# Kernel optimization log

Measured on AMD Instinct MI355X. Metric: run time of the kernel, lower is better.

The kernel has to match this reference:

```python
import jax, jax.numpy as jnp
import numpy as np

B, E, T = 8192, 512, 32


def setup_inputs() -> dict:
    key = jax.random.key(0)
    k1, k2, k3, k4, k5, k6 = jax.random.split(key, 6)
    s1 = 1.0 / np.sqrt(E)  # torch nn.Linear default init scale (uniform bound)
    return {
        "g_exp": jax.random.normal(k1, (B, E), dtype=jnp.float32),
        "tissue_vector": jax.random.randint(k2, (B, 1), 0, T, dtype=jnp.int64),
        # per-tissue head params: Linear(E,E) then Linear(E,1)
        "W1": jax.random.uniform(k3, (T, E, E), jnp.float32, -s1, s1),
        "b1": jax.random.uniform(k4, (T, E), jnp.float32, -s1, s1),
        "W2": jax.random.uniform(k5, (T, E), jnp.float32, -s1, s1),
        "b2": jax.random.uniform(k6, (T,), jnp.float32, -s1, s1),
    }


def reference(g_exp, tissue_vector, W1, b1, W2, b2):
    # Each sample b is routed through the MLP head of its tissue id.
    # Vectorized: run every sample through every tissue head, then select.
    # h[b,t,:] = GELU(g_exp[b] @ W1[t] + b1[t])
    h = jax.nn.gelu(jnp.einsum("be,teh->bth", g_exp, W1) + b1[None, :, :],
                    approximate=False)  # exact erf GELU, matches torch nn.GELU
    # y[b,t] = softplus(h[b,t] @ W2[t] + b2[t])   (Softplus since loss_fn='poisson')
    y = jax.nn.softplus(jnp.einsum("bth,th->bt", h, W2) + b2[None, :])
    tid = tissue_vector[:, 0]  # [B], tissue id per sample
    return jnp.take_along_axis(y, tid[:, None], axis=1)  # [B, 1]
```

## Files before the change

kernel.cpp:

```cpp
#include <hip/hip_runtime.h>
#include <math.h>

#define B_N 8192
#define E_N 512
#define T_N 32
#define DEPTH 5

typedef short bf16x8 __attribute__((ext_vector_type(8)));
typedef float f32x4 __attribute__((ext_vector_type(4)));

#define WS_OFFS   256
#define WS_RANK   512
#define WS_ORDER  33280
#define WS_YACC   66048
#define WS_ABF    98816
#define WS_W1T    (WS_ABF + 8388608)
#define WS_REQ    (WS_W1T + 33554432/2)

typedef __attribute__((address_space(1))) const unsigned int gas_u32;
typedef __attribute__((address_space(3))) unsigned int las_u32;

static __device__ __forceinline__ unsigned short f2bf(float f) {
    unsigned int u = __float_as_uint(f);
    unsigned int r = u + 0x7fffu + ((u >> 16) & 1u);
    return (unsigned short)(r >> 16);
}

__global__ __launch_bounds__(256) void k_pre(
    const float* __restrict__ W1, unsigned short* __restrict__ W1T,
    const float* __restrict__ g_exp, unsigned short* __restrict__ Abf,
    const int* __restrict__ tv, int* __restrict__ offs_g,
    int* __restrict__ rank, int* __restrict__ order, float* __restrict__ yacc) {
    int cid = blockIdx.x, tid = threadIdx.x;
    if (cid < 2048) {
        __shared__ float T[64][65];
        int t = cid >> 6, r = cid & 63;
        int k0 = (r >> 3) * 64, n0 = (r & 7) * 64;
        int g = tid >> 4, c = tid & 15;
#pragma unroll
        for (int p = 0; p < 4; ++p) {
            int row = p * 16 + g;
            float4 v = *(const float4*)(W1 + ((size_t)t * E_N + k0 + row) * E_N + n0 + c * 4);
            T[c * 4 + 0][row] = v.x;
            T[c * 4 + 1][row] = v.y;
            T[c * 4 + 2][row] = v.z;
            T[c * 4 + 3][row] = v.w;
        }
        __syncthreads();
#pragma unroll
        for (int p = 0; p < 4; ++p) {
            int n = p * 16 + g;
            ushort4 o;
            o.x = f2bf(T[n][c * 4 + 0]);
            o.y = f2bf(T[n][c * 4 + 1]);
            o.z = f2bf(T[n][c * 4 + 2]);
            o.w = f2bf(T[n][c * 4 + 3]);
            *(ushort4*)(W1T + ((size_t)t * E_N + n0 + n) * E_N + k0 + c * 4) = o;
        }
    } else if (cid < 2304) {
        int b0 = (cid - 2048) * 32;
#pragma unroll 4
        for (int pp = 0; pp < 16; ++pp) {
            int idx = pp * 256 + tid;
            int row = idx >> 7, c = idx & 127;
            float4 v = *(const float4*)(g_exp + ((size_t)(b0 + row)) * E_N + c * 4);
            ushort4 o;
            o.x = f2bf(v.x); o.y = f2bf(v.y); o.z = f2bf(v.z); o.w = f2bf(v.w);
            *(ushort4*)(Abf + ((size_t)(b0 + row)) * E_N + c * 4) = o;
        }
    } else {
        __shared__ int lh[4][32], wcur[4][32], offs_s[33];
        int w = tid >> 6;
        if (tid < 128) lh[tid >> 5][tid & 31] = 0;
        __syncthreads();
        int tval[32];
#pragma unroll
        for (int c = 0; c < 32; ++c) tval[c] = tv[c * 256 + tid];
#pragma unroll
        for (int c = 0; c < 32; ++c) atomicAdd(&lh[w][tval[c]], 1);
        __syncthreads();
        if (tid < 32) {
            int s = lh[0][tid] + lh[1][tid] + lh[2][tid] + lh[3][tid];
            int excl = 0;
#pragma unroll
            for (int i = 0; i < 32; ++i) {
                int v = __shfl(s, i, 64);
                if (i < tid) excl += v;
            }
            offs_s[tid] = excl;
            offs_g[tid] = excl;
            if (tid == 31) { offs_s[32] = excl + s; offs_g[32] = excl + s; }
        }
        __syncthreads();
        if (tid < 128) {
            int ww = tid >> 5, t = tid & 31;
            int s = offs_s[t];
            for (int w2 = 0; w2 < ww; ++w2) s += lh[w2][t];
            wcur[ww][t] = s;
        }
        __syncthreads();
#pragma unroll
        for (int c = 0; c < 32; ++c) {
            int b = c * 256 + tid;
            int pos = atomicAdd(&wcur[w][tval[c]], 1);
            rank[b] = pos;
            order[pos] = b;
        }
        float4 z = make_float4(0.f, 0.f, 0.f, 0.f);
#pragma unroll
        for (int c = 0; c < 8; ++c) *(float4*)(yacc + (c * 256 + tid) * 4) = z;
    }
}

__global__ __launch_bounds__(256) void k_gemm_mfma(
    const unsigned short* __restrict__ Abf, const unsigned short* __restrict__ W1T,
    const float* __restrict__ b1, const float* __restrict__ W2,
    const int* __restrict__ offs, const int* __restrict__ order,
    float* __restrict__ yacc) {
    int wi = blockIdx.x;
    int mt = wi >> 7;
    int rem = wi & 127;
    int t = rem >> 2, nt = rem & 3;
    int base = offs[t];
    int n_t = offs[t + 1] - base;
    int m0 = mt * 128;
    if (m0 >= n_t) return;
    int n0 = nt * 128;

    __shared__ __align__(16) unsigned short As[DEPTH][128 * 32];
    __shared__ __align__(16) unsigned short Bs[DEPTH][128 * 32];

    int tid = threadIdx.x;
    int wave = tid >> 6, lane = tid & 63;
    int quad = lane >> 4, l15 = lane & 15;
    int wm = (wave >> 1) * 64, wn = (wave & 1) * 64;

    int idx0 = tid, idx1 = tid + 256;
    int r0 = idx0 >> 2;
    int kc = (idx0 & 3) ^ (r0 & 3);
    int r1 = r0 + 64;
    int i0 = base + m0 + r0; if (i0 > B_N - 1) i0 = B_N - 1;
    int i1 = base + m0 + r1; if (i1 > B_N - 1) i1 = B_N - 1;
    int o0 = order[i0], o1 = order[i1];
    const unsigned short* pA0 = Abf + (size_t)o0 * E_N + kc * 8;
    const unsigned short* pA1 = Abf + (size_t)o1 * E_N + kc * 8;
    const unsigned short* pB0 = W1T + ((size_t)t * E_N + n0 + r0) * E_N + kc * 8;
    const unsigned short* pB1 = W1T + ((size_t)t * E_N + n0 + r1) * E_N + kc * 8;

    f32x4 acc[4][4];
#pragma unroll
    for (int mi = 0; mi < 4; ++mi)
#pragma unroll
        for (int ni = 0; ni < 4; ++ni) acc[mi][ni] = (f32x4){0.f, 0.f, 0.f, 0.f};

#define ISSUE(kk) do {                                                                              \
        __builtin_amdgcn_global_load_lds((gas_u32*)(pB0 + (kk) * 32),                               \
                                         (las_u32*)&Bs[(kk) % DEPTH][idx0 * 8], 16, 0, 0);          \
        __builtin_amdgcn_global_load_lds((gas_u32*)(pB1 + (kk) * 32),                               \
                                         (las_u32*)&Bs[(kk) % DEPTH][idx1 * 8], 16, 0, 0);          \
        __builtin_amdgcn_global_load_lds((gas_u32*)(pA0 + (kk) * 32),                               \
                                         (las_u32*)&As[(kk) % DEPTH][idx0 * 8], 16, 0, 0);          \
        __builtin_amdgcn_global_load_lds((gas_u32*)(pA1 + (kk) * 32),                               \
                                         (las_u32*)&As[(kk) % DEPTH][idx1 * 8], 16, 0, 0);          \
    } while (0)

    ISSUE(0); ISSUE(1); ISSUE(2); ISSUE(3);

    int aoff[4], boff[4];
#pragma unroll
    for (int i = 0; i < 4; ++i) {
        aoff[i] = ((wm + i * 16 + l15) * 4 + (quad ^ (l15 & 3))) * 8;
        boff[i] = ((wn + i * 16 + l15) * 4 + (quad ^ (l15 & 3))) * 8;
    }

#define STAGE(it, W) do {                                                                           \
        asm volatile("s_waitcnt vmcnt(%0)" :: "n"(W) : "memory");                                   \
        asm volatile("s_barrier" ::: "memory");                                                     \
        const unsigned short* Ab = &As[(it) % DEPTH][0];                                            \
        const unsigned short* Bb = &Bs[(it) % DEPTH][0];                                            \
        bf16x8 af[4], bfr[4];                                                                       \
        _Pragma("unroll") for (int i = 0; i < 4; ++i) {                                             \
            af[i]  = *(const bf16x8*)(Ab + aoff[i]);                                                \
            bfr[i] = *(const bf16x8*)(Bb + boff[i]);                                                \
        }                                                                                           \
        _Pragma("unroll") for (int mi = 0; mi < 4; ++mi)                                            \
            _Pragma("unroll") for (int ni = 0; ni < 4; ++ni)                                        \
                acc[mi][ni] = __builtin_amdgcn_mfma_f32_16x16x32_bf16(af[mi], bfr[ni],              \
                                                                      acc[mi][ni], 0, 0, 0);        \
        if ((it) + 4 < 16) ISSUE((it) + 4);                                                         \
    } while (0)

    STAGE(0, 12);  STAGE(1, 12);  STAGE(2, 12);  STAGE(3, 12);
    STAGE(4, 12);  STAGE(5, 12);  STAGE(6, 12);  STAGE(7, 12);
    STAGE(8, 12);  STAGE(9, 12);  STAGE(10, 12); STAGE(11, 12);
    STAGE(12, 12); STAGE(13, 8);  STAGE(14, 4);  STAGE(15, 0);
#undef STAGE
#undef ISSUE

    float pr[4][4];
#pragma unroll
    for (int mi = 0; mi < 4; ++mi)
#pragma unroll
        for (int r = 0; r < 4; ++r) pr[mi][r] = 0.f;
#pragma unroll
    for (int ni = 0; ni < 4; ++ni) {
        int n = n0 + wn + ni * 16 + l15;
        float bb = b1[t * E_N + n];
        float w2 = W2[t * E_N + n];
#pragma unroll
        for (int mi = 0; mi < 4; ++mi)
#pragma unroll
            for (int r = 0; r < 4; ++r) {
                float u = acc[mi][ni][r] + bb;
                float gg = 0.5f * u * (1.f + erff(u * 0.70710678118654752f));
                pr[mi][r] = fmaf(gg, w2, pr[mi][r]);
            }
    }
#pragma unroll
    for (int off = 1; off <= 8; off <<= 1)
#pragma unroll
        for (int mi = 0; mi < 4; ++mi)
#pragma unroll
            for (int r = 0; r < 4; ++r) pr[mi][r] += __shfl_xor(pr[mi][r], off, 64);

    if (l15 == 0) {
#pragma unroll
        for (int mi = 0; mi < 4; ++mi)
#pragma unroll
            for (int r = 0; r < 4; ++r) {
                int row = m0 + wm + mi * 16 + quad * 4 + r;
                if (row < n_t) atomicAdd(&yacc[base + row], pr[mi][r]);
            }
    }
}

__global__ void k_final(const float* __restrict__ yacc, const int* __restrict__ rank,
                        const int* __restrict__ tv, const float* __restrict__ b2,
                        float* __restrict__ out, int use_rank) {
    int b = blockIdx.x * blockDim.x + threadIdx.x;
    if (b < B_N) {
        int idx = use_rank ? rank[b] : b;
        float x = yacc[idx] + b2[tv[b]];
        out[b] = fmaxf(x, 0.f) + log1pf(expf(-fabsf(x)));
    }
}

__global__ __launch_bounds__(256) void k_prep_sb(
    const int* __restrict__ tv, int* __restrict__ offs_g,
    int* __restrict__ rank, int* __restrict__ order, float* __restrict__ yacc) {
    __shared__ int lh[4][32], wcur[4][32], offs_s[33];
    int tid = threadIdx.x, w = tid >> 6;
    if (tid < 128) lh[tid >> 5][tid & 31] = 0;
    __syncthreads();
    int tval[32];
#pragma unroll
    for (int c = 0; c < 32; ++c) tval[c] = tv[c * 256 + tid];
#pragma unroll
    for (int c = 0; c < 32; ++c) atomicAdd(&lh[w][tval[c]], 1);
    __syncthreads();
    if (tid < 32) {
        int s = lh[0][tid] + lh[1][tid] + lh[2][tid] + lh[3][tid];
        int excl = 0;
#pragma unroll
        for (int i = 0; i < 32; ++i) {
            int v = __shfl(s, i, 64);
            if (i < tid) excl += v;
        }
        offs_s[tid] = excl;
        offs_g[tid] = excl;
        if (tid == 31) { offs_s[32] = excl + s; offs_g[32] = excl + s; }
    }
    __syncthreads();
    if (tid < 128) {
        int ww = tid >> 5, t = tid & 31;
        int s = offs_s[t];
        for (int w2 = 0; w2 < ww; ++w2) s += lh[w2][t];
        wcur[ww][t] = s;
    }
    __syncthreads();
#pragma unroll
    for (int c = 0; c < 32; ++c) {
        int b = c * 256 + tid;
        int pos = atomicAdd(&wcur[w][tval[c]], 1);
        rank[b] = pos;
        order[pos] = b;
    }
    float4 z = make_float4(0.f, 0.f, 0.f, 0.f);
#pragma unroll
    for (int c = 0; c < 8; ++c) *(float4*)(yacc + (c * 256 + tid) * 4) = z;
}

__global__ __launch_bounds__(256) void fb_gemm(
    const float* __restrict__ g_exp, const float* __restrict__ W1,
    const float* __restrict__ b1, const float* __restrict__ W2,
    const int* __restrict__ offs, const int* __restrict__ order,
    float* __restrict__ yacc) {
    int t = blockIdx.z;
    int base = offs[t];
    int n_t = offs[t + 1] - base;
    int m0 = blockIdx.y * 64;
    if (m0 >= n_t) return;
    int n0 = blockIdx.x * 128;

    __shared__ float As[32][68];
    __shared__ float Bs[32][128];
    __shared__ int sidx[64];

    int tid = threadIdx.x;
    if (tid < 64) {
        int m = m0 + tid;
        sidx[tid] = (m < n_t) ? order[base + m] : -1;
    }
    __syncthreads();

    int ty = tid >> 4, tx = tid & 15;
    float acc[4][8];
#pragma unroll
    for (int r = 0; r < 4; ++r)
#pragma unroll
        for (int c = 0; c < 8; ++c) acc[r][c] = 0.f;

    for (int k0 = 0; k0 < E_N; k0 += 32) {
#pragma unroll
        for (int p = 0; p < 2; ++p) {
            int idx = tid + 256 * p;
            int row = idx >> 3, kcq = idx & 7;
            int s = sidx[row];
            float4 v = make_float4(0.f, 0.f, 0.f, 0.f);
            if (s >= 0) v = *(const float4*)(g_exp + (size_t)s * E_N + k0 + kcq * 4);
            As[kcq * 4 + 0][row] = v.x;
            As[kcq * 4 + 1][row] = v.y;
            As[kcq * 4 + 2][row] = v.z;
            As[kcq * 4 + 3][row] = v.w;
        }
#pragma unroll
        for (int p = 0; p < 4; ++p) {
            int idx = tid + 256 * p;
            int kr = idx >> 5, c4 = idx & 31;
            *(float4*)(&Bs[kr][c4 * 4]) =
                *(const float4*)(W1 + ((size_t)t * E_N + (k0 + kr)) * E_N + n0 + c4 * 4);
        }
        __syncthreads();
#pragma unroll
        for (int e = 0; e < 32; ++e) {
            float4 a = *(const float4*)(&As[e][ty * 4]);
            float4 bA = *(const float4*)(&Bs[e][tx * 4]);
            float4 bB = *(const float4*)(&Bs[e][tx * 4 + 64]);
            float av[4] = {a.x, a.y, a.z, a.w};
            float bv[8] = {bA.x, bA.y, bA.z, bA.w, bB.x, bB.y, bB.z, bB.w};
#pragma unroll
            for (int r = 0; r < 4; ++r)
#pragma unroll
                for (int c = 0; c < 8; ++c) acc[r][c] = fmaf(av[r], bv[c], acc[r][c]);
        }
        __syncthreads();
    }

    float pr[4] = {0.f, 0.f, 0.f, 0.f};
#pragma unroll
    for (int c = 0; c < 8; ++c) {
        int n = n0 + tx * 4 + ((c >= 4) ? 64 : 0) + (c & 3);
        float bb = b1[t * E_N + n];
        float w2 = W2[t * E_N + n];
#pragma unroll
        for (int r = 0; r < 4; ++r) {
            float u = acc[r][c] + bb;
            float g = 0.5f * u * (1.f + erff(u * 0.70710678118654752f));
            pr[r] = fmaf(g, w2, pr[r]);
        }
    }
#pragma unroll
    for (int off = 8; off >= 1; off >>= 1)
#pragma unroll
        for (int r = 0; r < 4; ++r) pr[r] += __shfl_xor(pr[r], off, 64);

    if (tx == 0) {
#pragma unroll
        for (int r = 0; r < 4; ++r) {
            int m = m0 + ty * 4 + r;
            if (m < n_t) atomicAdd(&yacc[sidx[ty * 4 + r]], pr[r]);
        }
    }
}

extern "C" void kernel_launch(void* const* d_in, const int* in_sizes, int n_in,
                              void* d_out, int out_size, void* d_ws, size_t ws_size,
                              hipStream_t stream) {
    const float* g_exp = (const float*)d_in[0];
    const int*   tv    = (const int*)d_in[1];
    const float* W1    = (const float*)d_in[2];
    const float* b1    = (const float*)d_in[3];
    const float* W2    = (const float*)d_in[4];
    const float* b2    = (const float*)d_in[5];
    float* out = (float*)d_out;

    char* ws = (char*)d_ws;
    int* offs   = (int*)(ws + WS_OFFS);
    int* rank   = (int*)(ws + WS_RANK);
    int* order  = (int*)(ws + WS_ORDER);
    float* yacc = (float*)(ws + WS_YACC);

    if (ws_size >= (size_t)WS_REQ) {
        unsigned short* Abf = (unsigned short*)(ws + WS_ABF);
        unsigned short* W1T = (unsigned short*)(ws + WS_W1T);
        k_pre<<<2305, 256, 0, stream>>>(W1, W1T, g_exp, Abf, tv, offs, rank, order, yacc);
        k_gemm_mfma<<<512, 256, 0, stream>>>(Abf, W1T, b1, W2, offs, order, yacc);
        k_final<<<32, 256, 0, stream>>>(yacc, rank, tv, b2, out, 1);
    } else {
        k_prep_sb<<<1, 256, 0, stream>>>(tv, offs, rank, order, yacc);
        fb_gemm<<<dim3(4, 8, 32), 256, 0, stream>>>(g_exp, W1, b1, W2, offs, order, yacc);
        k_final<<<32, 256, 0, stream>>>(yacc, rank, tv, b2, out, 0);
    }
}
```

Measured before the change: 133.3 us.

## Fuse activation bf16 conversion and tissue routing into the MFMA GEMM kernel

Removes the separate g_exp-to-bf16 conversion and the single-block histogram/sort stage from the preprocess kernel. Each GEMM block now counts its tissue's rows from tv itself, builds the row list in LDS, loads fp32 activations straight into LDS and converts them to bf16 when reading MFMA fragments. Per-column partial sums go to eight per-slab buffers with plain stores instead of atomics, and the final kernel reduces them, so the yacc zeroing is no longer needed. In exchange every block rescans all 8192 tissue ids, the A tile doubles in size (fp32), and pipeline depth drops from 5 to 3 buffers.

```diff
diff --git a/kernel.cpp b/kernel.cpp
--- a/kernel.cpp
+++ b/kernel.cpp
@@ -1,10 +1,10 @@
 #include <hip/hip_runtime.h>
+#include <hip/hip_bf16.h>
 #include <math.h>
 
 #define B_N 8192
 #define E_N 512
 #define T_N 32
-#define DEPTH 5
 
 typedef short bf16x8 __attribute__((ext_vector_type(8)));
 typedef float f32x4 __attribute__((ext_vector_type(4)));
@@ -13,9 +13,9 @@
 #define WS_RANK   512
 #define WS_ORDER  33280
 #define WS_YACC   66048
-#define WS_ABF    98816
-#define WS_W1T    (WS_ABF + 8388608)
-#define WS_REQ    (WS_W1T + 33554432/2)
+#define WS_YACC8  98816
+#define WS_W1T    360960
+#define WS_REQ    (WS_W1T + 16777216)
 
 typedef __attribute__((address_space(1))) const unsigned int gas_u32;
 typedef __attribute__((address_space(3))) unsigned int las_u32;
@@ -26,126 +26,103 @@
     return (unsigned short)(r >> 16);
 }
 
-__global__ __launch_bounds__(256) void k_pre(
-    const float* __restrict__ W1, unsigned short* __restrict__ W1T,
-    const float* __restrict__ g_exp, unsigned short* __restrict__ Abf,
-    const int* __restrict__ tv, int* __restrict__ offs_g,
-    int* __restrict__ rank, int* __restrict__ order, float* __restrict__ yacc) {
+static __device__ __forceinline__ unsigned int pk2(float a, float b) {
+    __hip_bfloat162 h = __float22bfloat162_rn(float2{a, b});
+    unsigned int u;
+    __builtin_memcpy(&u, &h, 4);
+    return u;
+}
+
+__global__ __launch_bounds__(256) void k_pre(const float* __restrict__ W1,
+                                             unsigned short* __restrict__ W1T) {
+    __shared__ float T[64][65];
     int cid = blockIdx.x, tid = threadIdx.x;
-    if (cid < 2048) {
-        __shared__ float T[64][65];
-        int t = cid >> 6, r = cid & 63;
-        int k0 = (r >> 3) * 64, n0 = (r & 7) * 64;
-        int g = tid >> 4, c = tid & 15;
-#pragma unroll
-        for (int p = 0; p < 4; ++p) {
-            int row = p * 16 + g;
-            float4 v = *(const float4*)(W1 + ((size_t)t * E_N + k0 + row) * E_N + n0 + c * 4);
-            T[c * 4 + 0][row] = v.x;
-            T[c * 4 + 1][row] = v.y;
-            T[c * 4 + 2][row] = v.z;
-            T[c * 4 + 3][row] = v.w;
-        }
-        __syncthreads();
-#pragma unroll
-        for (int p = 0; p < 4; ++p) {
-            int n = p * 16 + g;
-            ushort4 o;
-            o.x = f2bf(T[n][c * 4 + 0]);
-            o.y = f2bf(T[n][c * 4 + 1]);
-            o.z = f2bf(T[n][c * 4 + 2]);
-            o.w = f2bf(T[n][c * 4 + 3]);
-            *(ushort4*)(W1T + ((size_t)t * E_N + n0 + n) * E_N + k0 + c * 4) = o;
-        }
-    } else if (cid < 2304) {
-        int b0 = (cid - 2048) * 32;
-#pragma unroll 4
-        for (int pp = 0; pp < 16; ++pp) {
-            int idx = pp * 256 + tid;
-            int row = idx >> 7, c = idx & 127;
-            float4 v = *(const float4*)(g_exp + ((size_t)(b0 + row)) * E_N + c * 4);
-            ushort4 o;
-            o.x = f2bf(v.x); o.y = f2bf(v.y); o.z = f2bf(v.z); o.w = f2bf(v.w);
-            *(ushort4*)(Abf + ((size_t)(b0 + row)) * E_N + c * 4) = o;
-        }
-    } else {
-        __shared__ int lh[4][32], wcur[4][32], offs_s[33];
-        int w = tid >> 6;
-        if (tid < 128) lh[tid >> 5][tid & 31] = 0;
-        __syncthreads();
-        int tval[32];
-#pragma unroll
-        for (int c = 0; c < 32; ++c) tval[c] = tv[c * 256 + tid];
-#pragma unroll
-        for (int c = 0; c < 32; ++c) atomicAdd(&lh[w][tval[c]], 1);
-        __syncthreads();
-        if (tid < 32) {
-            int s = lh[0][tid] + lh[1][tid] + lh[2][tid] + lh[3][tid];
-            int excl = 0;
-#pragma unroll
-            for (int i = 0; i < 32; ++i) {
-                int v = __shfl(s, i, 64);
-                if (i < tid) excl += v;
-            }
-            offs_s[tid] = excl;
-            offs_g[tid] = excl;
-            if (tid == 31) { offs_s[32] = excl + s; offs_g[32] = excl + s; }
-        }
-        __syncthreads();
-        if (tid < 128) {
-            int ww = tid >> 5, t = tid & 31;
-            int s = offs_s[t];
-            for (int w2 = 0; w2 < ww; ++w2) s += lh[w2][t];
-            wcur[ww][t] = s;
-        }
-        __syncthreads();
-#pragma unroll
-        for (int c = 0; c < 32; ++c) {
-            int b = c * 256 + tid;
-            int pos = atomicAdd(&wcur[w][tval[c]], 1);
-            rank[b] = pos;
-            order[pos] = b;
-        }
-        float4 z = make_float4(0.f, 0.f, 0.f, 0.f);
-#pragma unroll
-        for (int c = 0; c < 8; ++c) *(float4*)(yacc + (c * 256 + tid) * 4) = z;
+    int t = cid >> 6, r = cid & 63;
+    int k0 = (r >> 3) * 64, n0 = (r & 7) * 64;
+    int g = tid >> 4, c = tid & 15;
+#pragma unroll
+    for (int p = 0; p < 4; ++p) {
+        int row = p * 16 + g;
+        float4 v = *(const float4*)(W1 + ((size_t)t * E_N + k0 + row) * E_N + n0 + c * 4);
+        T[c * 4 + 0][row] = v.x;
+        T[c * 4 + 1][row] = v.y;
+        T[c * 4 + 2][row] = v.z;
+        T[c * 4 + 3][row] = v.w;
+    }
+    __syncthreads();
+#pragma unroll
+    for (int p = 0; p < 4; ++p) {
+        int n = p * 16 + g;
+        ushort4 o;
+        o.x = f2bf(T[n][c * 4 + 0]);
+        o.y = f2bf(T[n][c * 4 + 1]);
+        o.z = f2bf(T[n][c * 4 + 2]);
+        o.w = f2bf(T[n][c * 4 + 3]);
+        *(ushort4*)(W1T + ((size_t)t * E_N + n0 + n) * E_N + k0 + c * 4) = o;
     }
 }
 
 __global__ __launch_bounds__(256) void k_gemm_mfma(
-    const unsigned short* __restrict__ Abf, const unsigned short* __restrict__ W1T,
-    const float* __restrict__ b1, const float* __restrict__ W2,
-    const int* __restrict__ offs, const int* __restrict__ order,
-    float* __restrict__ yacc) {
+    const float* __restrict__ g_exp, const unsigned short* __restrict__ W1T,
+    const int* __restrict__ tv, const float* __restrict__ b1,
+    const float* __restrict__ W2, float* __restrict__ yacc8) {
     int wi = blockIdx.x;
     int mt = wi >> 7;
     int rem = wi & 127;
     int t = rem >> 2, nt = rem & 3;
-    int base = offs[t];
-    int n_t = offs[t + 1] - base;
-    int m0 = mt * 128;
-    if (m0 >= n_t) return;
-    int n0 = nt * 128;
-
-    __shared__ __align__(16) unsigned short As[DEPTH][128 * 32];
-    __shared__ __align__(16) unsigned short Bs[DEPTH][128 * 32];
+    int m0 = mt * 128, n0 = nt * 128;
 
     int tid = threadIdx.x;
     int wave = tid >> 6, lane = tid & 63;
     int quad = lane >> 4, l15 = lane & 15;
     int wm = (wave >> 1) * 64, wn = (wave & 1) * 64;
 
-    int idx0 = tid, idx1 = tid + 256;
-    int r0 = idx0 >> 2;
-    int kc = (idx0 & 3) ^ (r0 & 3);
-    int r1 = r0 + 64;
-    int i0 = base + m0 + r0; if (i0 > B_N - 1) i0 = B_N - 1;
-    int i1 = base + m0 + r1; if (i1 > B_N - 1) i1 = B_N - 1;
-    int o0 = order[i0], o1 = order[i1];
-    const unsigned short* pA0 = Abf + (size_t)o0 * E_N + kc * 8;
-    const unsigned short* pA1 = Abf + (size_t)o1 * E_N + kc * 8;
-    const unsigned short* pB0 = W1T + ((size_t)t * E_N + n0 + r0) * E_N + kc * 8;
-    const unsigned short* pB1 = W1T + ((size_t)t * E_N + n0 + r1) * E_N + kc * 8;
+    __shared__ int wsum[4];
+    __shared__ int rows_s[128];
+
+    int tvals[32];
+    const int4* tvp = (const int4*)(tv + tid * 32);
+#pragma unroll
+    for (int j = 0; j < 8; ++j) ((int4*)tvals)[j] = tvp[j];
+    int myc = 0;
+#pragma unroll
+    for (int j = 0; j < 32; ++j) myc += (tvals[j] == t) ? 1 : 0;
+    int inc = myc;
+#pragma unroll
+    for (int o = 1; o < 64; o <<= 1) {
+        int u = __shfl_up(inc, o, 64);
+        if (lane >= o) inc += u;
+    }
+    if (lane == 63) wsum[wave] = inc;
+    if (tid < 128) rows_s[tid] = 0;
+    __syncthreads();
+    int n_t = wsum[0] + wsum[1] + wsum[2] + wsum[3];
+    if (m0 >= n_t) return;
+    int wbase = 0;
+    for (int i = 0; i < wave; ++i) wbase += wsum[i];
+    int rk = wbase + inc - myc;
+#pragma unroll
+    for (int j = 0; j < 32; ++j)
+        if (tvals[j] == t) {
+            int rr = rk++;
+            if (rr >= m0 && rr < m0 + 128) rows_s[rr - m0] = tid * 32 + j;
+        }
+    __syncthreads();
+
+    const unsigned short* Bsrc = W1T + ((size_t)t * E_N + n0) * E_N;
+    int bd0 = tid, bd1 = tid + 256;
+    int brow0 = bd0 >> 2, bkc = (bd0 & 3) ^ (brow0 & 3);
+    const unsigned short* pB0 = Bsrc + (size_t)brow0 * E_N + bkc * 8;
+    const unsigned short* pB1 = Bsrc + (size_t)(brow0 + 64) * E_N + bkc * 8;
+    const float* pA[4];
+#pragma unroll
+    for (int p = 0; p < 4; ++p) {
+        int d = tid + 256 * p, arow = d >> 3, akc = (d & 7) ^ (arow & 7);
+        pA[p] = g_exp + (size_t)rows_s[arow] * E_N + akc * 4;
+    }
+
+    __shared__ __align__(16) float As[3][128 * 32];
+    __shared__ __align__(16) unsigned short Bsh[3][128 * 32];
 
     f32x4 acc[4][4];
 #pragma unroll
@@ -153,47 +130,49 @@
 #pragma unroll
         for (int ni = 0; ni < 4; ++ni) acc[mi][ni] = (f32x4){0.f, 0.f, 0.f, 0.f};
 
-#define ISSUE(kk) do {                                                                              \
-        __builtin_amdgcn_global_load_lds((gas_u32*)(pB0 + (kk) * 32),                               \
-                                         (las_u32*)&Bs[(kk) % DEPTH][idx0 * 8], 16, 0, 0);          \
-        __builtin_amdgcn_global_load_lds((gas_u32*)(pB1 + (kk) * 32),                               \
-                                         (las_u32*)&Bs[(kk) % DEPTH][idx1 * 8], 16, 0, 0);          \
-        __builtin_amdgcn_global_load_lds((gas_u32*)(pA0 + (kk) * 32),                               \
-                                         (las_u32*)&As[(kk) % DEPTH][idx0 * 8], 16, 0, 0);          \
-        __builtin_amdgcn_global_load_lds((gas_u32*)(pA1 + (kk) * 32),                               \
-                                         (las_u32*)&As[(kk) % DEPTH][idx1 * 8], 16, 0, 0);          \
+#define ISSUE(kk) do {                                                                         \
+        int _ko = (kk) * 32;                                                                   \
+        __builtin_amdgcn_global_load_lds((gas_u32*)(pB0 + _ko),                                \
+                                         (las_u32*)&Bsh[(kk) % 3][bd0 * 8], 16, 0, 0);         \
+        __builtin_amdgcn_global_load_lds((gas_u32*)(pB1 + _ko),                                \
+                                         (las_u32*)&Bsh[(kk) % 3][bd1 * 8], 16, 0, 0);         \
+        _Pragma("unroll") for (int p = 0; p < 4; ++p)                                          \
+            __builtin_amdgcn_global_load_lds((gas_u32*)(pA[p] + _ko),                          \
+                                             (las_u32*)&As[(kk) % 3][(tid + 256 * p) * 4],     \
+                                             16, 0, 0);                                        \
     } while (0)
 
-    ISSUE(0); ISSUE(1); ISSUE(2); ISSUE(3);
-
-    int aoff[4], boff[4];
-#pragma unroll
-    for (int i = 0; i < 4; ++i) {
-        aoff[i] = ((wm + i * 16 + l15) * 4 + (quad ^ (l15 & 3))) * 8;
-        boff[i] = ((wn + i * 16 + l15) * 4 + (quad ^ (l15 & 3))) * 8;
-    }
-
-#define STAGE(it, W) do {                                                                           \
-        asm volatile("s_waitcnt vmcnt(%0)" :: "n"(W) : "memory");                                   \
-        asm volatile("s_barrier" ::: "memory");                                                     \
-        const unsigned short* Ab = &As[(it) % DEPTH][0];                                            \
-        const unsigned short* Bb = &Bs[(it) % DEPTH][0];                                            \
-        bf16x8 af[4], bfr[4];                                                                       \
-        _Pragma("unroll") for (int i = 0; i < 4; ++i) {                                             \
-            af[i]  = *(const bf16x8*)(Ab + aoff[i]);                                                \
-            bfr[i] = *(const bf16x8*)(Bb + boff[i]);                                                \
-        }                                                                                           \
-        _Pragma("unroll") for (int mi = 0; mi < 4; ++mi)                                            \
-            _Pragma("unroll") for (int ni = 0; ni < 4; ++ni)                                        \
-                acc[mi][ni] = __builtin_amdgcn_mfma_f32_16x16x32_bf16(af[mi], bfr[ni],              \
-                                                                      acc[mi][ni], 0, 0, 0);        \
-        if ((it) + 4 < 16) ISSUE((it) + 4);                                                         \
+    ISSUE(0);
+    ISSUE(1);
+
+#define STAGE(it, W) do {                                                                      \
+        asm volatile("s_waitcnt vmcnt(%0)" :: "n"(W) : "memory");                              \
+        asm volatile("s_barrier" ::: "memory");                                                \
+        const float* Ab = &As[(it) % 3][0];                                                    \
+        const unsigned short* Bb = &Bsh[(it) % 3][0];                                          \
+        bf16x8 af[4], bfr[4];                                                                  \
+        _Pragma("unroll") for (int i = 0; i < 4; ++i) {                                        \
+            int arow = wm + i * 16 + l15;                                                      \
+            int c0 = (quad * 2) ^ (arow & 7), c1 = (quad * 2 + 1) ^ (arow & 7);                \
+            f32x4 lo = *(const f32x4*)(Ab + arow * 32 + c0 * 4);                               \
+            f32x4 hi = *(const f32x4*)(Ab + arow * 32 + c1 * 4);                               \
+            unsigned int uu[4] = {pk2(lo[0], lo[1]), pk2(lo[2], lo[3]),                        \
+                                  pk2(hi[0], hi[1]), pk2(hi[2], hi[3])};                       \
+            __builtin_memcpy(&af[i], uu, 16);                                                  \
+            int brow = wn + i * 16 + l15;                                                      \
+            bfr[i] = *(const bf16x8*)(Bb + (brow * 4 + (quad ^ (l15 & 3))) * 8);               \
+        }                                                                                      \
+        _Pragma("unroll") for (int mi = 0; mi < 4; ++mi)                                       \
+            _Pragma("unroll") for (int ni = 0; ni < 4; ++ni)                                   \
+                acc[mi][ni] = __builtin_amdgcn_mfma_f32_16x16x32_bf16(af[mi], bfr[ni],         \
+                                                                      acc[mi][ni], 0, 0, 0);   \
+        if ((it) + 2 < 16) ISSUE((it) + 2);                                                    \
     } while (0)
 
-    STAGE(0, 12);  STAGE(1, 12);  STAGE(2, 12);  STAGE(3, 12);
-    STAGE(4, 12);  STAGE(5, 12);  STAGE(6, 12);  STAGE(7, 12);
-    STAGE(8, 12);  STAGE(9, 12);  STAGE(10, 12); STAGE(11, 12);
-    STAGE(12, 12); STAGE(13, 8);  STAGE(14, 4);  STAGE(15, 0);
+    STAGE(0, 6);  STAGE(1, 6);  STAGE(2, 6);  STAGE(3, 6);
+    STAGE(4, 6);  STAGE(5, 6);  STAGE(6, 6);  STAGE(7, 6);
+    STAGE(8, 6);  STAGE(9, 6);  STAGE(10, 6); STAGE(11, 6);
+    STAGE(12, 6); STAGE(13, 6); STAGE(14, 6); STAGE(15, 0);
 #undef STAGE
 #undef ISSUE
 
@@ -224,23 +203,24 @@
             for (int r = 0; r < 4; ++r) pr[mi][r] += __shfl_xor(pr[mi][r], off, 64);
 
     if (l15 == 0) {
+        float* slab = yacc8 + (size_t)(nt * 2 + (wave & 1)) * B_N;
 #pragma unroll
         for (int mi = 0; mi < 4; ++mi)
 #pragma unroll
             for (int r = 0; r < 4; ++r) {
-                int row = m0 + wm + mi * 16 + quad * 4 + r;
-                if (row < n_t) atomicAdd(&yacc[base + row], pr[mi][r]);
+                int rl = wm + mi * 16 + quad * 4 + r;
+                if (m0 + rl < n_t) slab[rows_s[rl]] = pr[mi][r];
             }
     }
 }
 
-__global__ void k_final(const float* __restrict__ yacc, const int* __restrict__ rank,
-                        const int* __restrict__ tv, const float* __restrict__ b2,
-                        float* __restrict__ out, int use_rank) {
+__global__ void k_final8(const float* __restrict__ yacc8, const int* __restrict__ tv,
+                         const float* __restrict__ b2, float* __restrict__ out) {
     int b = blockIdx.x * blockDim.x + threadIdx.x;
     if (b < B_N) {
-        int idx = use_rank ? rank[b] : b;
-        float x = yacc[idx] + b2[tv[b]];
+        float x = b2[tv[b]];
+#pragma unroll
+        for (int s = 0; s < 8; ++s) x += yacc8[(size_t)s * B_N + b];
         out[b] = fmaxf(x, 0.f) + log1pf(expf(-fabsf(x)));
     }
 }
@@ -383,6 +363,15 @@
     }
 }
 
+__global__ void fb_final(const float* __restrict__ yacc, const int* __restrict__ tv,
+                         const float* __restrict__ b2, float* __restrict__ out) {
+    int b = blockIdx.x * blockDim.x + threadIdx.x;
+    if (b < B_N) {
+        float x = yacc[b] + b2[tv[b]];
+        out[b] = fmaxf(x, 0.f) + log1pf(expf(-fabsf(x)));
+    }
+}
+
 extern "C" void kernel_launch(void* const* d_in, const int* in_sizes, int n_in,
                               void* d_out, int out_size, void* d_ws, size_t ws_size,
                               hipStream_t stream) {
@@ -395,20 +384,20 @@
     float* out = (float*)d_out;
 
     char* ws = (char*)d_ws;
-    int* offs   = (int*)(ws + WS_OFFS);
-    int* rank   = (int*)(ws + WS_RANK);
-    int* order  = (int*)(ws + WS_ORDER);
-    float* yacc = (float*)(ws + WS_YACC);
 
     if (ws_size >= (size_t)WS_REQ) {
-        unsigned short* Abf = (unsigned short*)(ws + WS_ABF);
+        float* yacc8 = (float*)(ws + WS_YACC8);
         unsigned short* W1T = (unsigned short*)(ws + WS_W1T);
-        k_pre<<<2305, 256, 0, stream>>>(W1, W1T, g_exp, Abf, tv, offs, rank, order, yacc);
-        k_gemm_mfma<<<512, 256, 0, stream>>>(Abf, W1T, b1, W2, offs, order, yacc);
-        k_final<<<32, 256, 0, stream>>>(yacc, rank, tv, b2, out, 1);
+        k_pre<<<2048, 256, 0, stream>>>(W1, W1T);
+        k_gemm_mfma<<<512, 256, 0, stream>>>(g_exp, W1T, tv, b1, W2, yacc8);
+        k_final8<<<32, 256, 0, stream>>>(yacc8, tv, b2, out);
     } else {
+        int* offs   = (int*)(ws + WS_OFFS);
+        int* rank   = (int*)(ws + WS_RANK);
+        int* order  = (int*)(ws + WS_ORDER);
+        float* yacc = (float*)(ws + WS_YACC);
         k_prep_sb<<<1, 256, 0, stream>>>(tv, offs, rank, order, yacc);
         fb_gemm<<<dim3(4, 8, 32), 256, 0, stream>>>(g_exp, W1, b1, W2, offs, order, yacc);
-        k_final<<<32, 256, 0, stream>>>(yacc, rank, tv, b2, out, 0);
-    }
-}
+        fb_final<<<32, 256, 0, stream>>>(yacc, tv, b2, out);
+    }
+}
```

After: 135.9 us. No clear change (+1.9%).
